# Optimization experiments

Measured on AMD Instinct MI355X. Metric: run time of the kernel, lower is better.

Reference implementation:

```python
import jax, jax.numpy as jnp
import numpy as np
from jax import lax

B, C, H, W = 32, 512, 32, 32
NH = 8
ER = 4
DK_RATIO = 0.2
EPS_LN = 1e-6


def _layernorm(t, g, b):
    m = t.mean(-1, keepdims=True)
    v = ((t - m) ** 2).mean(-1, keepdims=True)
    return (t - m) / jnp.sqrt(v + EPS_LN) * g + b


def setup_inputs() -> dict:
    key = jax.random.key(0)
    ks = jax.random.split(key, 24)
    s = 0.02
    dh = C // NH
    return {
        "x": jax.random.normal(ks[0], (B, C, H, W), jnp.float32),
        "mask_u": jax.random.uniform(ks[1], (B, NH, dh, dh), jnp.float32),
        "dw_w": jax.random.normal(ks[2], (C, 1, 3, 3), jnp.float32) * s,
        "dw_b": jnp.zeros((C,), jnp.float32),
        "ln1_g": jnp.ones((C,), jnp.float32),
        "ln1_b": jnp.zeros((C,), jnp.float32),
        "qkv_w": jax.random.normal(ks[3], (3 * C, C), jnp.float32) * s,
        "qkv_b": jnp.zeros((3 * C,), jnp.float32),
        "temp": jnp.ones((NH, 1, 1), jnp.float32),
        "proj_w": jax.random.normal(ks[4], (C, C), jnp.float32) * s,
        "proj_b": jnp.zeros((C,), jnp.float32),
        "ct_w": jax.random.normal(ks[5], (C, C, 2, 2), jnp.float32) * s,  # [in,out,kH,kW]
        "ct_b": jnp.zeros((C,), jnp.float32),
        "ln2_g": jnp.ones((C,), jnp.float32),
        "ln2_b": jnp.zeros((C,), jnp.float32),
        "pw1_w": jax.random.normal(ks[6], (ER * C, C), jnp.float32) * s,
        "pw1_b": jnp.zeros((ER * C,), jnp.float32),
        "pw2_w": jax.random.normal(ks[7], (C, ER * C), jnp.float32) * s,
        "pw2_b": jnp.zeros((C,), jnp.float32),
    }


def reference(x, mask_u, dw_w, dw_b, ln1_g, ln1_b, qkv_w, qkv_b, temp,
              proj_w, proj_b, ct_w, ct_b, ln2_g, ln2_b,
              pw1_w, pw1_b, pw2_w, pw2_b):
    inp = x
    b, c, h, w = x.shape
    # depthwise 3x3 conv + residual
    dw = lax.conv_general_dilated(
        x, dw_w, (1, 1), "SAME", feature_group_count=c,
        dimension_numbers=("NCHW", "OIHW", "NCHW")) + dw_b[None, :, None, None]
    x = dw + inp
    # 2x2 avg pool, stride 2
    hp, wp = h // 2, w // 2
    x = x.reshape(b, c, hp, 2, wp, 2).mean(axis=(3, 5))  # [B,C,hp,wp]
    n = hp * wp
    # tokens [B,N,C] -> LN -> qkv
    t = x.reshape(b, c, n).transpose(0, 2, 1)
    t = _layernorm(t, ln1_g, ln1_b)
    qkv = t @ qkv_w.T + qkv_b                       # [B,N,3C]
    dh = c // NH
    qkv = qkv.reshape(b, n, 3, NH, dh).transpose(2, 0, 3, 1, 4)  # [3,B,h,N,d]
    # cosine (XCA-style) attention: transpose to [B,h,d,N], normalize over N
    q = jnp.swapaxes(qkv[0], -2, -1)
    k = jnp.swapaxes(qkv[1], -2, -1)
    v = jnp.swapaxes(qkv[2], -2, -1)
    q = q / jnp.maximum(jnp.linalg.norm(q, axis=-1, keepdims=True), 1e-12)
    k = k / jnp.maximum(jnp.linalg.norm(k, axis=-1, keepdims=True), 1e-12)
    attn = jnp.einsum("bhdn,bhen->bhde", q, k) * temp  # [B,h,d,d]
    attn = attn + (mask_u < DK_RATIO).astype(attn.dtype) * (-1e12)
    attn = jax.nn.softmax(attn, axis=-1)
    out = jnp.einsum("bhde,bhen->bhdn", attn, v)       # [B,h,d,N]
    out = out.transpose(0, 3, 1, 2).reshape(b, n, c)
    t = out @ proj_w.T + proj_b
    t = t + t
    x = t.transpose(0, 2, 1).reshape(b, c, hp, wp)
    # ConvTranspose2d(C,C,2,stride=2): each pixel expands to 2x2 block
    x = jnp.einsum("bchw,copq->bohpwq", x, ct_w).reshape(b, c, 2 * hp, 2 * wp)
    x = x + ct_b[None, :, None, None]
    # MLP in channels-last
    y = x.transpose(0, 2, 3, 1)                        # [B,H,W,C]
    y = _layernorm(y, ln2_g, ln2_b)
    y = jax.nn.gelu(y @ pw1_w.T + pw1_b, approximate=False)
    y = y @ pw2_w.T + pw2_b
    x = y.transpose(0, 3, 1, 2)
    return inp + x
```

## Files before the change

kernel.cpp:

```cpp
#include <hip/hip_runtime.h>
#include <hip/hip_bf16.h>
#include <math.h>

typedef unsigned short ushort;
typedef __attribute__((ext_vector_type(8))) short short8;
typedef __attribute__((ext_vector_type(8))) unsigned short ushort8;
typedef __attribute__((ext_vector_type(4))) unsigned short ushort4v;
typedef __attribute__((ext_vector_type(4))) float f32x4;

__device__ __forceinline__ ushort f2bb(float v) {
    return __builtin_bit_cast(ushort, __float2bfloat16(v));
}
__device__ __forceinline__ float bf2f(ushort u) {
    return __bfloat162float(__builtin_bit_cast(__hip_bfloat16, u));
}
__device__ __forceinline__ void gl2lds16(const ushort* g, ushort* l) {
    __builtin_amdgcn_global_load_lds(
        (const __attribute__((address_space(1))) unsigned int*)g,
        (__attribute__((address_space(3))) unsigned int*)l, 16, 0, 0);
}


__global__ __launch_bounds__(256) void cvtw_k(const float* __restrict__ in,
                                              ushort* __restrict__ out, int n4) {
    int i = blockIdx.x * 256 + threadIdx.x;
    if (i >= n4) return;
    float4 v = ((const float4*)in)[i];
    ushort4v o;
    o.x = f2bb(v.x); o.y = f2bb(v.y); o.z = f2bb(v.z); o.w = f2bb(v.w);
    ((ushort4v*)out)[i] = o;
}

__global__ __launch_bounds__(256) void cvtt_k(const float* __restrict__ in,
                                              ushort* __restrict__ out) {
    __shared__ float tl[32][33];
    int c0 = blockIdx.y * 32, j0 = blockIdx.x * 32;
    int tr = threadIdx.x >> 5, tc = threadIdx.x & 31;
#pragma unroll
    for (int p4 = 0; p4 < 4; ++p4)
        tl[tr + p4 * 8][tc] = in[(size_t)(c0 + tr + p4 * 8) * 2048 + j0 + tc];
    __syncthreads();
#pragma unroll
    for (int p4 = 0; p4 < 4; ++p4)
        out[(size_t)(j0 + tr + p4 * 8) * 512 + c0 + tc] = f2bb(tl[tc][tr + p4 * 8]);
}

__global__ __launch_bounds__(256) void dwpool_k(const float* __restrict__ x,
                                                const float* __restrict__ dww,
                                                const float* __restrict__ dwb,
                                                ushort* __restrict__ xp) {
    int bc = blockIdx.x;
    int c = bc & 511;
    __shared__ float tile[32][33];
    __shared__ float w9[9];
    const float* xb = x + (size_t)bc * 1024;
    int tid = threadIdx.x;
    for (int i = tid; i < 1024; i += 256) tile[i >> 5][i & 31] = xb[i];
    if (tid < 9) w9[tid] = dww[c * 9 + tid];
    __syncthreads();
    float bv = dwb[c];
    int ph = tid >> 4, pw = tid & 15;
    float s = 0.f;
#pragma unroll
    for (int dy = 0; dy < 2; ++dy) {
#pragma unroll
        for (int dx = 0; dx < 2; ++dx) {
            int hh = 2 * ph + dy, ww = 2 * pw + dx;
            float a = bv + tile[hh][ww];
#pragma unroll
            for (int ky = 0; ky < 3; ++ky) {
                int yy = hh + ky - 1;
                if (yy < 0 || yy > 31) continue;
#pragma unroll
                for (int kx = 0; kx < 3; ++kx) {
                    int xx = ww + kx - 1;
                    if (xx < 0 || xx > 31) continue;
                    a += w9[ky * 3 + kx] * tile[yy][xx];
                }
            }
            s += a;
        }
    }
    xp[(size_t)bc * 256 + tid] = f2bb(0.25f * s);
}

__global__ __launch_bounds__(256) void ln1_stats_k(const ushort* __restrict__ xp,
                                                   float* __restrict__ m1,
                                                   float* __restrict__ r1) {
    __shared__ float sh_s[4][64], sh_q[4][64];
    int blk = blockIdx.x;
    int b = blk >> 2;
    int n0 = (blk & 3) * 64;
    int t = threadIdx.x & 63, w = threadIdx.x >> 6;
    float s = 0.f, ss = 0.f;
    for (int i = 0; i < 128; ++i) {
        int c = w * 128 + i;
        float v = bf2f(xp[(size_t)(b * 512 + c) * 256 + n0 + t]);
        s += v; ss += v * v;
    }
    sh_s[w][t] = s; sh_q[w][t] = ss;
    __syncthreads();
    if (w == 0) {
        s  = sh_s[0][t] + sh_s[1][t] + sh_s[2][t] + sh_s[3][t];
        ss = sh_q[0][t] + sh_q[1][t] + sh_q[2][t] + sh_q[3][t];
        float m = s * (1.0f / 512.0f);
        m1[b * 256 + n0 + t] = m;
        r1[b * 256 + n0 + t] = rsqrtf(ss * (1.0f / 512.0f) - m * m + 1e-6f);
    }
}

__global__ __launch_bounds__(256) void ln1_apply_k(const ushort* __restrict__ xp,
                                                   const float* __restrict__ m1,
                                                   const float* __restrict__ r1,
                                                   const float* __restrict__ g,
                                                   const float* __restrict__ beta,
                                                   ushort* __restrict__ a_ln) {
    __shared__ float tl[64][66];
    int blk = blockIdx.x;
    int b = blk >> 5, ct = (blk >> 2) & 7, nt = blk & 3;
    int t = threadIdx.x;
    int rq = t >> 6, nl = t & 63;
#pragma unroll
    for (int i = 0; i < 16; ++i) {
        int r = rq * 16 + i;
        int c = ct * 64 + r;
        tl[r][nl] = bf2f(xp[(size_t)(b * 512 + c) * 256 + nt * 64 + nl]);
    }
    __syncthreads();
    int r2 = t >> 2, cq = t & 3;
    int m = b * 256 + nt * 64 + r2;
    float mu = m1[m], rs = r1[m];
#pragma unroll
    for (int hh = 0; hh < 2; ++hh) {
        ushort8 o;
#pragma unroll
        for (int j = 0; j < 8; ++j) {
            int cl = cq * 16 + hh * 8 + j;
            int c = ct * 64 + cl;
            o[j] = f2bb((tl[cl][r2] - mu) * rs * g[c] + beta[c]);
        }
        *(ushort8*)&a_ln[(size_t)m * 512 + ct * 64 + cq * 16 + hh * 8] = o;
    }
}

__global__ __launch_bounds__(256) void ln2_fuse_k(ushort* __restrict__ yB,
                                                  ushort* __restrict__ yT,
                                                  const float* __restrict__ g,
                                                  const float* __restrict__ beta) {
    int w = threadIdx.x >> 6, lane = threadIdx.x & 63;
    int row = blockIdx.x * 4 + w;
    ushort* base = (row < 8192) ? (yB + (size_t)row * 512)
                                : (yT + (size_t)(row - 8192) * 512);
    ushort8 raw = *(ushort8*)&base[lane * 8];
    float v[8];
    float s = 0.f, ss = 0.f;
#pragma unroll
    for (int j = 0; j < 8; ++j) { v[j] = bf2f(raw[j]); s += v[j]; ss += v[j] * v[j]; }
#pragma unroll
    for (int off = 1; off < 64; off <<= 1) { s += __shfl_xor(s, off); ss += __shfl_xor(ss, off); }
    float mu = s * (1.0f / 512.0f);
    float rs = rsqrtf(ss * (1.0f / 512.0f) - mu * mu + 1e-6f);
    ushort8 o;
#pragma unroll
    for (int j = 0; j < 8; ++j) {
        int c = lane * 8 + j;
        o[j] = f2bb((v[j] - mu) * rs * g[c] + beta[c]);
    }
    *(ushort8*)&base[lane * 8] = o;
}

struct GP {
    const ushort* A;
    const ushort* W;
    const float* bias;
    ushort* outB;
    ushort* outB2;
    float* outF;
    const float* inp;
    int K, m0;
};

template <int MODE, int BN>
__global__ __launch_bounds__(256) void mgemm_k(GP p) {
    constexpr int MT = (BN == 128) ? 4 : 2;
    constexpr int NT = 4;
    constexpr int ATILE = 128 * 32;
    constexpr int BTILE = BN * 32;
    constexpr int SMEM_US = 2 * (ATILE + BTILE);
    __shared__ __align__(16) ushort smem[SMEM_US];
    int tid = threadIdx.x;
    int lane = tid & 63, w = tid >> 6;
    int lr = lane & 15, lq = lane >> 4;
    int mwoff = (BN == 128) ? (w >> 1) * 64 : w * 32;
    int nwoff = (BN == 128) ? (w & 1) * 64 : 0;
    int gx = gridDim.x;
    int wgid = blockIdx.y * gx + blockIdx.x;
    int cpx = (gx * gridDim.y) >> 3;
    int swz = (wgid & 7) * cpx + (wgid >> 3);
    int bx = swz % gx, by = swz / gx;
    int mbase = by * 128, nbase = bx * BN;
    int lsub = lane >> 2;
    int cchunk = (lane & 3) ^ ((lsub >> 1) & 3);
    int lcol = cchunk * 8;
    int physc = lq ^ ((lr >> 1) & 3);
    f32x4 acc[MT][NT] = {};

    auto stage = [&](int buf, int kb) {
        ushort* Ab = smem + buf * ATILE;
        ushort* Bb = smem + 2 * ATILE + buf * BTILE;
#pragma unroll
        for (int i = 0; i < 2; ++i) {
            int row = w * 32 + i * 16;
            gl2lds16(p.A + (size_t)(mbase + row + lsub) * p.K + kb + lcol,
                     &Ab[row * 32]);
        }
        if constexpr (BN == 128) {
#pragma unroll
            for (int i = 0; i < 2; ++i) {
                int row = w * 32 + i * 16;
                gl2lds16(p.W + (size_t)(nbase + row + lsub) * p.K + kb + lcol,
                         &Bb[row * 32]);
            }
        } else {
            int row = w * 16;
            gl2lds16(p.W + (size_t)(nbase + row + lsub) * p.K + kb + lcol,
                     &Bb[row * 32]);
        }
    };

    stage(0, 0);
    __syncthreads();
    int nk = p.K >> 5;
    for (int t = 0; t < nk; ++t) {
        int cur = t & 1;
        if (t + 1 < nk) stage(cur ^ 1, (t + 1) << 5);
        const ushort* Ac = smem + cur * ATILE;
        const ushort* Bc = smem + 2 * ATILE + cur * BTILE;
        short8 af[MT], bfr[NT];
#pragma unroll
        for (int tt = 0; tt < MT; ++tt)
            af[tt] = *(const short8*)&Ac[(mwoff + tt * 16 + lr) * 32 + physc * 8];
#pragma unroll
        for (int tt = 0; tt < NT; ++tt)
            bfr[tt] = *(const short8*)&Bc[(nwoff + tt * 16 + lr) * 32 + physc * 8];
#pragma unroll
        for (int i = 0; i < MT; ++i)
#pragma unroll
            for (int j = 0; j < NT; ++j)
                acc[i][j] = __builtin_amdgcn_mfma_f32_16x16x32_bf16(af[i], bfr[j], acc[i][j], 0, 0, 0);
        __syncthreads();
    }

    if constexpr (MODE == 1 || MODE == 3) {
        const size_t LD = (MODE == 1) ? 512 : 2048;
        ushort* eb = (ushort*)smem;
#pragma unroll
        for (int h = 0; h < 2; ++h) {
            __syncthreads();
            if ((w & 1) == h) {
#pragma unroll
                for (int ti = 0; ti < MT; ++ti)
#pragma unroll
                    for (int tj = 0; tj < NT; ++tj)
#pragma unroll
                        for (int r = 0; r < 4; ++r) {
                            int row = mwoff + ti * 16 + lq * 4 + r;
                            int colh = tj * 16 + lr;
                            float v = acc[ti][tj][r] + p.bias[nbase + h * 64 + colh];
                            if constexpr (MODE == 1) v *= 2.0f;
                            else v = 0.5f * v * (1.0f + erff(v * 0.70710678118654752f));
                            int ph = (colh >> 3) ^ (row & 7);
                            eb[row * 64 + ph * 8 + (colh & 7)] = f2bb(v);
                        }
            }
            __syncthreads();
#pragma unroll
            for (int i = 0; i < 4; ++i) {
                int row = i * 32 + (tid >> 3);
                int ch = tid & 7;
                int pch = ch ^ (row & 7);
                short8 d = *(short8*)&eb[row * 64 + pch * 8];
                *(short8*)&p.outB[(size_t)(mbase + row) * LD + nbase + h * 64 + ch * 8] = d;
            }
        }
    } else if constexpr (MODE == 0) {
        ushort* eb = (ushort*)smem;
        int b = mbase >> 8, n0 = mbase & 255;
#pragma unroll
        for (int pc = 0; pc < 4; ++pc) {
            __syncthreads();
            if ((w & 1) == (pc >> 1)) {
                int tjb = (pc & 1) * 2;
#pragma unroll
                for (int ti = 0; ti < MT; ++ti)
#pragma unroll
                    for (int tj2 = 0; tj2 < 2; ++tj2)
#pragma unroll
                        for (int r = 0; r < 4; ++r) {
                            int tj = tjb + tj2;
                            int row = mwoff + ti * 16 + lq * 4 + r;
                            int cl = tj2 * 16 + lr;
                            float v = acc[ti][tj][r] + p.bias[nbase + pc * 32 + cl];
                            eb[cl * 136 + row] = f2bb(v);
                        }
            }
            __syncthreads();
            if (nbase < 1024) {
#pragma unroll
                for (int i = 0; i < 2; ++i) {
                    int dl = (tid >> 4) + 16 * i;
                    int ch = tid & 15;
                    short8 d = *(short8*)&eb[dl * 136 + ch * 8];
                    int cg = nbase + pc * 32 + dl;
                    int sect = cg >> 9, hh = (cg >> 6) & 7, dd = cg & 63;
                    size_t addr = ((size_t)(sect * 256 + b * 8 + hh) * 64 + dd) * 256 + n0 + ch * 8;
                    *(short8*)&p.outB[addr] = d;
                }
            } else {
                int cv = nbase + pc * 32 - 1024;
                int bh2 = b * 8 + (cv >> 6);
                int d0 = cv & 63;
#pragma unroll
                for (int i = 0; i < 2; ++i) {
                    int idx = i * 256 + tid;
                    int n = idx >> 2, oc = idx & 3;
                    ushort8 dv;
#pragma unroll
                    for (int j = 0; j < 8; ++j) dv[j] = eb[(oc * 8 + j) * 136 + n];
                    *(ushort8*)&p.outB[(size_t)8388608 + (size_t)bh2 * 16384 +
                                       (size_t)(n0 + n) * 64 + d0 + oc * 8] = dv;
                }
            }
        }
    } else if constexpr (MODE == 2) {
        ushort* eb = (ushort*)smem;
        ushort* ybase = (mbase < 2048) ? p.outB : (p.outB2 - (size_t)8192 * 512);
        int obase = nbase >> 2;
#pragma unroll
        for (int hf = 0; hf < 2; ++hf) {
            __syncthreads();
            if ((w >> 1) == hf) {
#pragma unroll
                for (int ti = 0; ti < MT; ++ti)
#pragma unroll
                    for (int tj = 0; tj < NT; ++tj)
#pragma unroll
                        for (int r = 0; r < 4; ++r) {
                            int rl = (mwoff - hf * 64) + ti * 16 + lq * 4 + r;
                            int cgl = nwoff + tj * 16 + lr;
                            int o_l = cgl >> 2, pp = (cgl >> 1) & 1, qq = cgl & 1;
                            int pix = ((rl >> 4) * 2 + pp) * 32 + (rl & 15) * 2 + qq;
                            float v = acc[ti][tj][r] + p.bias[obase + o_l];
                            eb[pix * 40 + o_l] = f2bb(v);
                        }
            }
            __syncthreads();
            int hhbase = ((mbase & 255) >> 4) + hf * 4;
            int prb = (mbase >> 8) * 32 + 2 * hhbase;
#pragma unroll
            for (int i = 0; i < 4; ++i) {
                int pix = i * 64 + (tid >> 2);
                int ch = tid & 3;
                short8 d = *(short8*)&eb[pix * 40 + ch * 8];
                int pr = (prb + (pix >> 5)) * 32 + (pix & 31);
                *(short8*)&ybase[(size_t)pr * 512 + obase + ch * 8] = d;
            }
        }
    }
}

__global__ __launch_bounds__(512) void mlp_fused_k(
    const ushort* __restrict__ yB, const ushort* __restrict__ yT,
    const ushort* __restrict__ w1, const ushort* __restrict__ w2,
    const float* __restrict__ b1, const float* __restrict__ b2,
    const float* __restrict__ inp, float* __restrict__ outF) {
    __shared__ __align__(16) ushort Asm[64 * 512];
    __shared__ __align__(16) ushort Hsm[64 * 256];
    int tid = threadIdx.x;
    int lane = tid & 63, w = tid >> 6;
    int lr = lane & 15, lq = lane >> 4;
    int wgid = blockIdx.x;
    int swz = (wgid & 7) * 64 + (wgid >> 3);
    int mbase = swz * 64;
    const ushort* yb = (mbase < 8192) ? (yB + (size_t)mbase * 512)
                                      : (yT + (size_t)(mbase - 8192) * 512);
#pragma unroll
    for (int j = 0; j < 8; ++j) {
        int row = w * 8 + j;
        int sc = lane ^ (row & 7);
        gl2lds16(yb + (size_t)row * 512 + sc * 8, &Asm[row * 512]);
    }
    int ocol0 = w * 64;
    int hcol0 = w * 32;
    float b2v[4];
#pragma unroll
    for (int nt = 0; nt < 4; ++nt) b2v[nt] = b2[ocol0 + nt * 16 + lr];
    asm volatile("s_waitcnt vmcnt(0)" ::: "memory");
    __syncthreads();

    f32x4 acc2[4][4] = {};
#pragma unroll 1
    for (int hb = 0; hb < 8; ++hb) {
        f32x4 acc1[4][2] = {};
#pragma unroll
        for (int kh = 0; kh < 16; ++kh) {
            short8 bf1[2];
#pragma unroll
            for (int nt = 0; nt < 2; ++nt)
                bf1[nt] = *(const short8*)&w1[(size_t)(hb * 256 + hcol0 + nt * 16 + lr) * 512 + kh * 32 + lq * 8];
#pragma unroll
            for (int mt = 0; mt < 4; ++mt) {
                int row = mt * 16 + lr;
                int c = kh * 4 + lq;
                short8 af = *(const short8*)&Asm[row * 512 + ((c ^ (row & 7)) << 3)];
#pragma unroll
                for (int nt = 0; nt < 2; ++nt)
                    acc1[mt][nt] = __builtin_amdgcn_mfma_f32_16x16x32_bf16(af, bf1[nt], acc1[mt][nt], 0, 0, 0);
            }
        }
        __syncthreads();
#pragma unroll
        for (int mt = 0; mt < 4; ++mt)
#pragma unroll
            for (int nt = 0; nt < 2; ++nt)
#pragma unroll
                for (int r = 0; r < 4; ++r) {
                    int row = mt * 16 + lq * 4 + r;
                    int hl = hcol0 + nt * 16 + lr;
                    float v = acc1[mt][nt][r] + b1[hb * 256 + hl];
                    v = 0.5f * v * (1.0f + erff(v * 0.70710678118654752f));
                    int c = hl >> 3;
                    Hsm[row * 256 + ((c ^ (row & 7)) << 3) + (hl & 7)] = f2bb(v);
                }
        __syncthreads();
#pragma unroll
        for (int kh = 0; kh < 8; ++kh) {
            short8 bf2[4];
#pragma unroll
            for (int nt = 0; nt < 4; ++nt)
                bf2[nt] = *(const short8*)&w2[(size_t)(ocol0 + nt * 16 + lr) * 2048 + hb * 256 + kh * 32 + lq * 8];
#pragma unroll
            for (int mt = 0; mt < 4; ++mt) {
                int row = mt * 16 + lr;
                int c = kh * 4 + lq;
                short8 ha = *(const short8*)&Hsm[row * 256 + ((c ^ (row & 7)) << 3)];
#pragma unroll
                for (int nt = 0; nt < 4; ++nt)
                    acc2[mt][nt] = __builtin_amdgcn_mfma_f32_16x16x32_bf16(ha, bf2[nt], acc2[mt][nt], 0, 0, 0);
            }
        }
    }
    int b = mbase >> 10;
    int hwb = mbase & 1023;
#pragma unroll
    for (int mt = 0; mt < 4; ++mt) {
#pragma unroll
        for (int nt = 0; nt < 4; ++nt) {
            int col = ocol0 + nt * 16 + lr;
            size_t idx = ((size_t)(b * 512 + col)) * 1024 + hwb + mt * 16 + lq * 4;
            float4 xin = *(const float4*)&inp[idx];
            float4 o4;
            o4.x = xin.x + acc2[mt][nt][0] + b2v[nt];
            o4.y = xin.y + acc2[mt][nt][1] + b2v[nt];
            o4.z = xin.z + acc2[mt][nt][2] + b2v[nt];
            o4.w = xin.w + acc2[mt][nt][3] + b2v[nt];
            *(float4*)&outF[idx] = o4;
        }
    }
}

__global__ __launch_bounds__(256) void attn_k(const ushort* __restrict__ qkvp,
                                              const float* __restrict__ mask_u,
                                              const float* __restrict__ temp,
                                              ushort* __restrict__ attn_out) {
    __shared__ float Sb[64 * 65];
    __shared__ ushort Pb[64 * 64];
    __shared__ float fq[64], fk[64];
    int tid = threadIdx.x;
    int bh = blockIdx.x;
    int b = bh >> 3, h = bh & 7;
    const ushort* q  = qkvp + (size_t)bh * 16384;
    const ushort* k  = qkvp + 4194304 + (size_t)bh * 16384;
    const ushort* vt = qkvp + 8388608 + (size_t)bh * 16384;
    int lane = tid & 63, w = tid >> 6;
    int lr = lane & 15, lq = lane >> 4;

    {
        int row = tid >> 2, qd = tid & 3;
        const ushort* qr = q + row * 256 + qd * 64;
        const ushort* kr = k + row * 256 + qd * 64;
        float s = 0.f, t = 0.f;
#pragma unroll
        for (int i = 0; i < 8; ++i) {
            short8 a8 = *(const short8*)&qr[i * 8];
            short8 b8 = *(const short8*)&kr[i * 8];
#pragma unroll
            for (int j = 0; j < 8; ++j) {
                float fa = bf2f((ushort)a8[j]); s += fa * fa;
                float fb = bf2f((ushort)b8[j]); t += fb * fb;
            }
        }
        s += __shfl_xor(s, 1); s += __shfl_xor(s, 2);
        t += __shfl_xor(t, 1); t += __shfl_xor(t, 2);
        if (qd == 0) {
            fq[row] = 1.0f / fmaxf(sqrtf(s), 1e-12f);
            fk[row] = 1.0f / fmaxf(sqrtf(t), 1e-12f);
        }
    }
    __syncthreads();

    int mq = (w >> 1) * 32, nq = (w & 1) * 32;
    f32x4 acc[2][2] = {};
    for (int kb = 0; kb < 256; kb += 32) {
        short8 af[2], bfr[2];
#pragma unroll
        for (int ti = 0; ti < 2; ++ti)
            af[ti] = *(const short8*)&q[(mq + ti * 16 + lr) * 256 + kb + lq * 8];
#pragma unroll
        for (int tj = 0; tj < 2; ++tj)
            bfr[tj] = *(const short8*)&k[(nq + tj * 16 + lr) * 256 + kb + lq * 8];
#pragma unroll
        for (int i = 0; i < 2; ++i)
#pragma unroll
            for (int j = 0; j < 2; ++j)
                acc[i][j] = __builtin_amdgcn_mfma_f32_16x16x32_bf16(af[i], bfr[j], acc[i][j], 0, 0, 0);
    }

    float tv = temp[h];
#pragma unroll
    for (int i = 0; i < 2; ++i)
#pragma unroll
        for (int r = 0; r < 4; ++r) {
            int d = mq + i * 16 + lq * 4 + r;
#pragma unroll
            for (int j = 0; j < 2; ++j) {
                int e = nq + j * 16 + lr;
                float sc = acc[i][j][r] * fq[d] * fk[e] * tv;
                float mu = mask_u[((size_t)bh * 64 + d) * 64 + e];
                if (mu < 0.2f) sc -= 1e12f;
                Sb[d * 65 + e] = sc;
            }
        }
    __syncthreads();

    {
        int row = tid >> 2, sub = tid & 3;
        float ev[16];
        float mx = -INFINITY;
#pragma unroll
        for (int i = 0; i < 16; ++i) { float s = Sb[row * 65 + sub * 16 + i]; ev[i] = s; mx = fmaxf(mx, s); }
        mx = fmaxf(mx, __shfl_xor(mx, 1));
        mx = fmaxf(mx, __shfl_xor(mx, 2));
        float sum = 0.f;
#pragma unroll
        for (int i = 0; i < 16; ++i) { ev[i] = expf(ev[i] - mx); sum += ev[i]; }
        sum += __shfl_xor(sum, 1);
        sum += __shfl_xor(sum, 2);
        float inv = 1.0f / sum;
        unsigned int* Pb32 = (unsigned int*)Pb;
#pragma unroll
        for (int kk = 0; kk < 8; ++kk) {
            unsigned int lo = f2bb(ev[2 * kk] * inv);
            unsigned int hi = f2bb(ev[2 * kk + 1] * inv);
            int c8 = sub * 2 + (kk >> 2);
            int ph = c8 ^ (row & 7);
            Pb32[row * 32 + ph * 4 + (kk & 3)] = (hi << 16) | lo;
        }
    }
    __syncthreads();

    int nw = w * 64;
    f32x4 o[4][4] = {};
#pragma unroll
    for (int ks = 0; ks < 2; ++ks) {
        short8 pa[4];
#pragma unroll
        for (int mt = 0; mt < 4; ++mt) {
            int d = mt * 16 + lr;
            int ph = (ks * 4 + lq) ^ (d & 7);
            pa[mt] = *(const short8*)&Pb[d * 64 + ph * 8];
        }
#pragma unroll
        for (int nt = 0; nt < 4; ++nt) {
            short8 vb = *(const short8*)&vt[(size_t)(nw + nt * 16 + lr) * 64 + ks * 32 + lq * 8];
#pragma unroll
            for (int mt = 0; mt < 4; ++mt)
                o[mt][nt] = __builtin_amdgcn_mfma_f32_16x16x32_bf16(pa[mt], vb, o[mt][nt], 0, 0, 0);
        }
    }

#pragma unroll
    for (int mt = 0; mt < 4; ++mt) {
        int d0 = mt * 16 + lq * 4;
#pragma unroll
        for (int nt = 0; nt < 4; ++nt) {
            int n = nw + nt * 16 + lr;
            ushort4v ov;
#pragma unroll
            for (int r = 0; r < 4; ++r) ov[r] = f2bb(o[mt][nt][r]);
            *(ushort4v*)&attn_out[((size_t)(b * 256 + n)) * 512 + h * 64 + d0] = ov;
        }
    }
}

extern "C" void kernel_launch(void* const* d_in, const int* in_sizes, int n_in,
                              void* d_out, int out_size, void* d_ws, size_t ws_size,
                              hipStream_t stream) {
    const float* x      = (const float*)d_in[0];
    const float* mask_u = (const float*)d_in[1];
    const float* dw_w   = (const float*)d_in[2];
    const float* dw_b   = (const float*)d_in[3];
    const float* ln1_g  = (const float*)d_in[4];
    const float* ln1_b  = (const float*)d_in[5];
    const float* qkv_w  = (const float*)d_in[6];
    const float* qkv_b  = (const float*)d_in[7];
    const float* temp   = (const float*)d_in[8];
    const float* proj_w = (const float*)d_in[9];
    const float* proj_b = (const float*)d_in[10];
    const float* ct_w   = (const float*)d_in[11];
    const float* ct_b   = (const float*)d_in[12];
    const float* ln2_g  = (const float*)d_in[13];
    const float* ln2_b  = (const float*)d_in[14];
    const float* pw1_w  = (const float*)d_in[15];
    const float* pw1_b  = (const float*)d_in[16];
    const float* pw2_w  = (const float*)d_in[17];
    const float* pw2_b  = (const float*)d_in[18];

    char* wsb = (char*)d_ws;
    float* mean1 = (float*)wsb;
    float* rstd1 = mean1 + 8192;
    ushort* wq = (ushort*)(wsb + 524288);
    ushort* wp = wq + 786432;
    ushort* wc = wp + 262144;
    ushort* w1 = wc + 1048576;
    ushort* w2 = w1 + 1048576;
    ushort* xp     = (ushort*)(wsb + 8912896);
    ushort* t2     = xp;
    ushort* a_ln   = (ushort*)(wsb + 17301504);
    ushort* yB     = a_ln;
    ushort* qkvp   = (ushort*)(wsb + 25690112);
    ushort* attn_o = (ushort*)(wsb + 50855936);
    ushort* yT     = (ushort*)(wsb + 59244544);

    cvtw_k<<<768,  256, 0, stream>>>(qkv_w,  wq, 196608);
    cvtw_k<<<256,  256, 0, stream>>>(proj_w, wp, 65536);
    cvtw_k<<<1024, 256, 0, stream>>>(pw1_w,  w1, 262144);
    cvtw_k<<<1024, 256, 0, stream>>>(pw2_w,  w2, 262144);
    cvtt_k<<<dim3(64, 16), 256, 0, stream>>>(ct_w, wc);
    dwpool_k<<<32 * 512, 256, 0, stream>>>(x, dw_w, dw_b, xp);
    ln1_stats_k<<<128, 256, 0, stream>>>(xp, mean1, rstd1);
    ln1_apply_k<<<1024, 256, 0, stream>>>(xp, mean1, rstd1, ln1_g, ln1_b, a_ln);
    {
        GP p{}; p.A = a_ln; p.W = wq; p.bias = qkv_b; p.outB = qkvp; p.K = 512;
        mgemm_k<0, 128><<<dim3(12, 64), 256, 0, stream>>>(p);
    }
    attn_k<<<256, 256, 0, stream>>>(qkvp, mask_u, temp, attn_o);
    {
        GP p{}; p.A = attn_o; p.W = wp; p.bias = proj_b; p.outB = t2; p.K = 512;
        mgemm_k<1, 128><<<dim3(4, 64), 256, 0, stream>>>(p);
    }
    {
        GP p{}; p.A = t2; p.W = wc; p.bias = ct_b;
        p.outB = yB; p.outB2 = yT; p.K = 512;
        mgemm_k<2, 128><<<dim3(16, 64), 256, 0, stream>>>(p);
    }
    ln2_fuse_k<<<8192, 256, 0, stream>>>(yB, yT, ln2_g, ln2_b);
    mlp_fused_k<<<512, 512, 0, stream>>>(yB, yT, w1, w2, pw1_b, pw2_b,
                                         x, (float*)d_out);
}
```

Measured before the change: 589.6 us.

## Halve hidden chunk in fused MLP and transpose first MFMA for vector H stores

The fused MLP kernel now processes the 2048-wide hidden dimension in 16 chunks of 128 instead of 8 chunks of 256. This halves the hidden-activation LDS buffer and the first-GEMM accumulators, and launch_bounds is set to (512, 4) to push more waves per CU. The first MFMA swaps operand order so each lane holds 4 consecutive hidden values, allowing a float4 bias load and a 4-wide packed bf16 store into LDS. The cost is twice as many block-wide barrier pairs and shorter inner loops per chunk.

```diff
diff --git a/kernel.cpp b/kernel.cpp
--- a/kernel.cpp
+++ b/kernel.cpp
@@ -369,13 +369,13 @@
     }
 }
 
-__global__ __launch_bounds__(512) void mlp_fused_k(
+__global__ __launch_bounds__(512, 4) void mlp_fused_k(
     const ushort* __restrict__ yB, const ushort* __restrict__ yT,
     const ushort* __restrict__ w1, const ushort* __restrict__ w2,
     const float* __restrict__ b1, const float* __restrict__ b2,
     const float* __restrict__ inp, float* __restrict__ outF) {
     __shared__ __align__(16) ushort Asm[64 * 512];
-    __shared__ __align__(16) ushort Hsm[64 * 256];
+    __shared__ __align__(16) ushort Hsm[64 * 128];
     int tid = threadIdx.x;
     int lane = tid & 63, w = tid >> 6;
     int lr = lane & 15, lq = lane >> 4;
@@ -391,7 +391,7 @@
         gl2lds16(yb + (size_t)row * 512 + sc * 8, &Asm[row * 512]);
     }
     int ocol0 = w * 64;
-    int hcol0 = w * 32;
+    int hcol0 = w * 16;
     float b2v[4];
 #pragma unroll
     for (int nt = 0; nt < 4; ++nt) b2v[nt] = b2[ocol0 + nt * 16 + lr];
@@ -400,53 +400,50 @@
 
     f32x4 acc2[4][4] = {};
 #pragma unroll 1
-    for (int hb = 0; hb < 8; ++hb) {
-        f32x4 acc1[4][2] = {};
+    for (int hb = 0; hb < 16; ++hb) {
+        f32x4 acc1[4] = {};
 #pragma unroll
         for (int kh = 0; kh < 16; ++kh) {
-            short8 bf1[2];
-#pragma unroll
-            for (int nt = 0; nt < 2; ++nt)
-                bf1[nt] = *(const short8*)&w1[(size_t)(hb * 256 + hcol0 + nt * 16 + lr) * 512 + kh * 32 + lq * 8];
+            short8 bf1 = *(const short8*)&w1[(size_t)(hb * 128 + hcol0 + lr) * 512 + kh * 32 + lq * 8];
 #pragma unroll
             for (int mt = 0; mt < 4; ++mt) {
                 int row = mt * 16 + lr;
                 int c = kh * 4 + lq;
                 short8 af = *(const short8*)&Asm[row * 512 + ((c ^ (row & 7)) << 3)];
-#pragma unroll
-                for (int nt = 0; nt < 2; ++nt)
-                    acc1[mt][nt] = __builtin_amdgcn_mfma_f32_16x16x32_bf16(af, bf1[nt], acc1[mt][nt], 0, 0, 0);
+                acc1[mt] = __builtin_amdgcn_mfma_f32_16x16x32_bf16(bf1, af, acc1[mt], 0, 0, 0);
             }
         }
         __syncthreads();
-#pragma unroll
-        for (int mt = 0; mt < 4; ++mt)
-#pragma unroll
-            for (int nt = 0; nt < 2; ++nt)
-#pragma unroll
-                for (int r = 0; r < 4; ++r) {
-                    int row = mt * 16 + lq * 4 + r;
-                    int hl = hcol0 + nt * 16 + lr;
-                    float v = acc1[mt][nt][r] + b1[hb * 256 + hl];
-                    v = 0.5f * v * (1.0f + erff(v * 0.70710678118654752f));
-                    int c = hl >> 3;
-                    Hsm[row * 256 + ((c ^ (row & 7)) << 3) + (hl & 7)] = f2bb(v);
-                }
+        int h0 = hcol0 + lq * 4;
+        float4 b1v = *(const float4*)&b1[hb * 128 + h0];
+#pragma unroll
+        for (int mt = 0; mt < 4; ++mt) {
+            int m = mt * 16 + lr;
+            ushort4v hv;
+#pragma unroll
+            for (int r = 0; r < 4; ++r) {
+                float v = acc1[mt][r] + ((const float*)&b1v)[r];
+                v = 0.5f * v * (1.0f + erff(v * 0.70710678118654752f));
+                hv[r] = f2bb(v);
+            }
+            int phys = (h0 >> 3) ^ (m & 7);
+            *(ushort4v*)&Hsm[m * 128 + (phys << 3) + (h0 & 7)] = hv;
+        }
         __syncthreads();
 #pragma unroll
-        for (int kh = 0; kh < 8; ++kh) {
-            short8 bf2[4];
+        for (int kh = 0; kh < 4; ++kh) {
+            short8 bf2v[4];
 #pragma unroll
             for (int nt = 0; nt < 4; ++nt)
-                bf2[nt] = *(const short8*)&w2[(size_t)(ocol0 + nt * 16 + lr) * 2048 + hb * 256 + kh * 32 + lq * 8];
+                bf2v[nt] = *(const short8*)&w2[(size_t)(ocol0 + nt * 16 + lr) * 2048 + hb * 128 + kh * 32 + lq * 8];
 #pragma unroll
             for (int mt = 0; mt < 4; ++mt) {
                 int row = mt * 16 + lr;
                 int c = kh * 4 + lq;
-                short8 ha = *(const short8*)&Hsm[row * 256 + ((c ^ (row & 7)) << 3)];
+                short8 ha = *(const short8*)&Hsm[row * 128 + ((c ^ (row & 7)) << 3)];
 #pragma unroll
                 for (int nt = 0; nt < 4; ++nt)
-                    acc2[mt][nt] = __builtin_amdgcn_mfma_f32_16x16x32_bf16(ha, bf2[nt], acc2[mt][nt], 0, 0, 0);
+                    acc2[mt][nt] = __builtin_amdgcn_mfma_f32_16x16x32_bf16(ha, bf2v[nt], acc2[mt][nt], 0, 0, 0);
             }
         }
     }
```

Measured after the change: 632.7 us. 7.3% more time.
